# Kernel optimization log

Measured on AMD Instinct MI355X. Metric: run time of the kernel, lower is better.

Reference implementation:

```python
import jax, jax.numpy as jnp
import numpy as np


def setup_inputs() -> dict:
    key = jax.random.key(0)
    k1, k2 = jax.random.split(key)
    B, N, D, OUT = 4, 8192, 64, 64
    inputs = jax.random.normal(k1, (B, N, D), dtype=jnp.float32)
    kernel = jax.random.normal(k2, (D, OUT), dtype=jnp.float32) * (1.0 / np.sqrt(D))
    return {"inputs": inputs, "kernel": kernel}


def reference(inputs, kernel):
    # sim = X X^T  -> [B, N, N] dense similarity (unscaled self-attention, V = X)
    sim = jnp.einsum("bnd,bmd->bnm", inputs, inputs)
    A = jax.nn.softmax(sim, axis=-1)          # row-wise softmax over neighbors
    h = jnp.einsum("bnm,bmd->bnd", A, inputs)  # aggregate
    return jnp.einsum("bnd,do->bno", h, kernel)  # output projection
```

## Files before the change

### kernel.cpp

```cpp
#include <hip/hip_runtime.h>
#include <math.h>

typedef _Float16 f16;
typedef _Float16 f16x2 __attribute__((ext_vector_type(2)));
typedef _Float16 f16x4 __attribute__((ext_vector_type(4)));
typedef _Float16 f16x8 __attribute__((ext_vector_type(8)));
typedef float    f32x4 __attribute__((ext_vector_type(4)));

#define PKRTZ(a, b) __builtin_bit_cast(f16x2, __builtin_amdgcn_cvt_pkrtz((a), (b)))

#define NN 8192
#define DD 64
#define KT 32
#define NQB 64
#define NWAVES 4
#define KPW (NN / NWAVES)
#define NTILES (KPW / KT)

#define LOG2E 1.44269504088896f

__global__ __launch_bounds__(256, 2)
void prep_f16(const float* __restrict__ X, f16* __restrict__ Xn, f16* __restrict__ Xv)
{
  __shared__ f16 Lt[64 * 72];
  const int tid  = threadIdx.x;
  const int b    = blockIdx.x >> 7;
  const int kb64 = (blockIdx.x & 127) * 64;

  {
    const int r = tid >> 2;
    const int c = (tid & 3) * 16;
    const float* p = X + ((size_t)(b * NN + kb64 + r)) * DD + c;
    const float4 a0 = *(const float4*)(p);
    const float4 a1 = *(const float4*)(p + 4);
    const float4 a2 = *(const float4*)(p + 8);
    const float4 a3 = *(const float4*)(p + 12);
    f16x8 v0, v1;
    v0[0]=(f16)a0.x; v0[1]=(f16)a0.y; v0[2]=(f16)a0.z; v0[3]=(f16)a0.w;
    v0[4]=(f16)a1.x; v0[5]=(f16)a1.y; v0[6]=(f16)a1.z; v0[7]=(f16)a1.w;
    v1[0]=(f16)a2.x; v1[1]=(f16)a2.y; v1[2]=(f16)a2.z; v1[3]=(f16)a2.w;
    v1[4]=(f16)a3.x; v1[5]=(f16)a3.y; v1[6]=(f16)a3.z; v1[7]=(f16)a3.w;
    f16* dn = Xn + ((size_t)(b * NN + kb64 + r)) * DD + c;
    *(f16x8*)(dn)     = v0;
    *(f16x8*)(dn + 8) = v1;
    *(f16x8*)&Lt[r * 72 + c]     = v0;
    *(f16x8*)&Lt[r * 72 + c + 8] = v1;
  }
  __syncthreads();
  {
    const int h  = tid >> 7;
    const int r  = tid & 127;
    const int jh = r & 1;
    const int d  = r >> 1;
    union { f16 s[16]; f16x8 v[2]; } u;
    #pragma unroll
    for (int j = 0; j < 16; ++j) u.s[j] = Lt[(h * 32 + jh * 16 + j) * 72 + d];
    const int kt = (kb64 >> 5) + h;
    f16* dst = Xv + (((size_t)(b * (NN / 32) + kt)) * DD + d) * 32 + jh * 16;
    *(f16x8*)&dst[0] = u.v[0];
    *(f16x8*)&dst[8] = u.v[1];
  }
}

#define P_PITCH 36
#define P_HALF  (64 * P_PITCH)
#define P_BYTES (2 * P_HALF * 2)
#define HL_PITCH 68
#define WL_OFF  (64 * HL_PITCH * 4)
#define LST_OFF (2 * 64 * HL_PITCH * 4)
#define SMEM_B  (NWAVES * P_BYTES)

__global__ __launch_bounds__(256, 2)
void gconv_attn(const float* __restrict__ X, const f16* __restrict__ Xn,
                const f16* __restrict__ Xv, const float* __restrict__ W,
                float* __restrict__ out)
{
  __shared__ __align__(16) unsigned char smem[SMEM_B];

  const int tid  = threadIdx.x;
  const int lane = tid & 63;
  const int wave = tid >> 6;
  const int q15  = lane & 15;
  const int quad = lane >> 4;

  const int xcd   = blockIdx.x & 7;
  const int slot  = blockIdx.x >> 3;
  const int batch = xcd >> 1;
  const int qblk  = slot * 2 + (xcd & 1);
  const int qbase = qblk * NQB;
  const float* Xb = X + (size_t)batch * NN * DD;

  f16* PwA = (f16*)(smem + wave * P_BYTES);
  f16* PwB = PwA + P_HALF;

  const f16* XnW = Xn + ((size_t)batch * NN + wave * KPW) * DD + q15 * DD + quad * 8;
  const f16* XvW = Xv + (((size_t)batch * (NN / 32) + wave * NTILES)) * DD * 32
                      + q15 * 32 + quad * 8;

  f16x8 qf[4][2];
  f32x4 minit[4];
  float lrow[4];
  #pragma unroll
  for (int qt = 0; qt < 4; ++qt) {
    const float* qp = Xb + (size_t)(qbase + qt*16 + q15) * DD + quad*8;
    float nrm = 0.f;
    #pragma unroll
    for (int c = 0; c < 2; ++c) {
      const float4 a = *(const float4*)(qp + c*32);
      const float4 b = *(const float4*)(qp + c*32 + 4);
      float xs[8] = {a.x, a.y, a.z, a.w, b.x, b.y, b.z, b.w};
      f16x8 v;
      #pragma unroll
      for (int e = 0; e < 8; ++e) {
        const f16 kv = (f16)xs[e];
        const f16 qs = (f16)(xs[e] * LOG2E);
        nrm += (float)qs * (float)kv;
        v[e] = qs;
      }
      qf[qt][c] = v;
    }
    nrm += __shfl_xor(nrm, 16);
    nrm += __shfl_xor(nrm, 32);
    const float m2 = nrm + 2.0f;
    minit[qt] = (f32x4){-m2, -m2, -m2, -m2};
    lrow[qt] = 0.f;
  }

  f32x4 acc[4][4];
  #pragma unroll
  for (int a = 0; a < 4; ++a)
    #pragma unroll
    for (int b = 0; b < 4; ++b)
      acc[a][b] = (f32x4){0.f, 0.f, 0.f, 0.f};

  const f16x2 kOnes = (f16x2){(f16)1.0f, (f16)1.0f};

  f16x8 ka[2][2], vbA[4], vbB[4];
  f32x4 sqk[4][2];

  auto LDK = [&](int t) {
    const f16* kn = XnW + (size_t)t * (KT * DD);
    #pragma unroll
    for (int g = 0; g < 2; ++g)
      #pragma unroll
      for (int c = 0; c < 2; ++c)
        ka[g][c] = *(const f16x8*)(kn + g * 16 * DD + c * 32);
  };
  auto LDV = [&](f16x8 (&vb)[4], int t) {
    const f16* vn = XvW + (size_t)t * (DD * 32);
    #pragma unroll
    for (int mt = 0; mt < 4; ++mt)
      vb[mt] = *(const f16x8*)(vn + mt * 16 * 32);
  };
  auto QK = [&]() {
    #pragma unroll
    for (int qt = 0; qt < 4; ++qt)
      #pragma unroll
      for (int g = 0; g < 2; ++g) {
        f32x4 s = __builtin_amdgcn_mfma_f32_16x16x32_f16(ka[g][0], qf[qt][0], minit[qt], 0, 0, 0);
        sqk[qt][g] = __builtin_amdgcn_mfma_f32_16x16x32_f16(ka[g][1], qf[qt][1], s, 0, 0, 0);
      }
  };
  auto SM = [&](f16* Pd) {
    #pragma unroll
    for (int qt = 0; qt < 4; ++qt)
      #pragma unroll
      for (int g = 0; g < 2; ++g) {
        const float p0 = __builtin_amdgcn_exp2f(sqk[qt][g][0]);
        const float p1 = __builtin_amdgcn_exp2f(sqk[qt][g][1]);
        const float p2 = __builtin_amdgcn_exp2f(sqk[qt][g][2]);
        const float p3 = __builtin_amdgcn_exp2f(sqk[qt][g][3]);
        union { f16x4 v; f16x2 h[2]; } pu;
        pu.h[0] = PKRTZ(p0, p1);
        pu.h[1] = PKRTZ(p2, p3);
        lrow[qt] = __builtin_amdgcn_fdot2(pu.h[0], kOnes, lrow[qt], false);
        lrow[qt] = __builtin_amdgcn_fdot2(pu.h[1], kOnes, lrow[qt], false);
        *(f16x4*)&Pd[(qt*16 + q15)*P_PITCH + g*16 + quad*4] = pu.v;
      }
  };
  auto PV = [&](const f16x8 (&vb)[4], const f16* Ps) {
    #pragma unroll
    for (int qt = 0; qt < 4; ++qt) {
      union { f16x8 v; f16x4 h[2]; } pu;
      pu.h[0] = *(const f16x4*)&Ps[(qt*16 + q15)*P_PITCH + quad*8];
      pu.h[1] = *(const f16x4*)&Ps[(qt*16 + q15)*P_PITCH + quad*8 + 4];
      #pragma unroll
      for (int mt = 0; mt < 4; ++mt)
        acc[qt][mt] = __builtin_amdgcn_mfma_f32_16x16x32_f16(vb[mt], pu.v, acc[qt][mt], 0, 0, 0);
    }
  };

  LDK(0);
  LDV(vbA, 0);
  QK();
  LDK(1);
  SM(PwA);
  LDV(vbB, 1);

  for (int t = 1; t < NTILES - 1; t += 2) {
    QK();
    LDK(t + 1);
    PV(vbA, PwA);
    LDV(vbA, t + 1);
    SM(PwB);
    QK();
    LDK(t + 2);
    PV(vbB, PwB);
    LDV(vbB, t + 2);
    SM(PwA);
  }

  QK();
  PV(vbA, PwA);
  SM(PwB);
  PV(vbB, PwB);

  __syncthreads();
  float* Hl    = (float*)smem;
  float* Wl    = (float*)(smem + WL_OFF);
  float* Lstar = (float*)(smem + LST_OFF);

  for (int i = tid; i < 64*HL_PITCH; i += 256) Hl[i] = 0.f;
  for (int i = tid; i < 64*64; i += 256) Wl[(i >> 6)*HL_PITCH + (i & 63)] = W[i];
  if (tid < 64) Lstar[tid] = 0.f;
  __syncthreads();

  #pragma unroll
  for (int qt = 0; qt < 4; ++qt) {
    float lr = lrow[qt];
    lr += __shfl_xor(lr, 16);
    lr += __shfl_xor(lr, 32);
    if (quad == 0) atomicAdd(&Lstar[qt*16 + q15], lr);
    #pragma unroll
    for (int mt = 0; mt < 4; ++mt)
      #pragma unroll
      for (int rr = 0; rr < 4; ++rr)
        atomicAdd(&Hl[(mt*16 + quad*4 + rr)*HL_PITCH + qt*16 + q15], acc[qt][mt][rr]);
  }
  __syncthreads();

  {
    const int qq = tid >> 2;
    const int og = (tid & 3) * 16;
    f32x4 o[4];
    #pragma unroll
    for (int i = 0; i < 4; ++i) o[i] = (f32x4){0.f,0.f,0.f,0.f};
    for (int d = 0; d < 64; ++d) {
      const float h = Hl[d*HL_PITCH + qq];
      const f32x4* wr = (const f32x4*)&Wl[d*HL_PITCH + og];
      #pragma unroll
      for (int i = 0; i < 4; ++i) o[i] += h * wr[i];
    }
    const float inv = 1.0f / Lstar[qq];
    float* op = out + ((size_t)batch * NN + qbase + qq) * DD + og;
    #pragma unroll
    for (int i = 0; i < 4; ++i)
      *(f32x4*)(op + i*4) = o[i] * inv;
  }
}

extern "C" void kernel_launch(void* const* d_in, const int* in_sizes, int n_in,
                              void* d_out, int out_size, void* d_ws, size_t ws_size,
                              hipStream_t stream) {
  const float* X = (const float*)d_in[0];
  const float* W = (const float*)d_in[1];
  float* out = (float*)d_out;

  f16* Xn = (f16*)d_ws;
  f16* Xv = (f16*)((char*)d_ws + (size_t)4 * NN * DD * 2);
  prep_f16<<<dim3(512), dim3(256), 0, stream>>>(X, Xn, Xv);
  gconv_attn<<<dim3(512), dim3(256), 0, stream>>>(X, Xn, Xv, W, out);
}
```

Baseline: 203.8 us.

## Switch attention to 32x32x16 MFMA and pass P in registers

The attention loop now uses 32x32x16 MFMA tiles instead of 16x16x32. The prep kernel permutes key rows within each 32-row group, so the QK^T output layout lines up with the A-operand layout of the PV MFMA. That lets the softmax probabilities feed the PV MFMA straight from registers, which removes the per-wave shared-memory P buffers and their LDS writes and reads. The explicit two-stage software pipeline is replaced by a simpler single-tile prefetch loop, which gives up some overlap between the QK, exp and PV phases. It also adds register pressure from the 16-wide accumulators under a 2-blocks-per-CU launch bound.

```diff
diff --git a/kernel.cpp b/kernel.cpp
--- a/kernel.cpp
+++ b/kernel.cpp
@@ -5,9 +5,11 @@
 typedef _Float16 f16x2 __attribute__((ext_vector_type(2)));
 typedef _Float16 f16x4 __attribute__((ext_vector_type(4)));
 typedef _Float16 f16x8 __attribute__((ext_vector_type(8)));
-typedef float    f32x4 __attribute__((ext_vector_type(4)));
+typedef float    f32x4  __attribute__((ext_vector_type(4)));
+typedef float    f32x16 __attribute__((ext_vector_type(16)));
 
 #define PKRTZ(a, b) __builtin_bit_cast(f16x2, __builtin_amdgcn_cvt_pkrtz((a), (b)))
+#define MFMA32(a, b, c) __builtin_amdgcn_mfma_f32_32x32x16_f16((a), (b), (c), 0, 0, 0)
 
 #define NN 8192
 #define DD 64
@@ -19,6 +21,11 @@
 
 #define LOG2E 1.44269504088896f
 
+__device__ __forceinline__ int sig32(int k) {
+  const int g = (k >> 2) & 3;
+  return (g == 1 || g == 2) ? (k ^ 12) : k;
+}
+
 __global__ __launch_bounds__(256, 2)
 void prep_f16(const float* __restrict__ X, f16* __restrict__ Xn, f16* __restrict__ Xv)
 {
@@ -28,8 +35,9 @@
   const int kb64 = (blockIdx.x & 127) * 64;
 
   {
-    const int r = tid >> 2;
-    const int c = (tid & 3) * 16;
+    const int r  = tid >> 2;
+    const int rr = (r & 32) | sig32(r & 31);
+    const int c  = (tid & 3) * 16;
     const float* p = X + ((size_t)(b * NN + kb64 + r)) * DD + c;
     const float4 a0 = *(const float4*)(p);
     const float4 a1 = *(const float4*)(p + 4);
@@ -40,7 +48,7 @@
     v0[4]=(f16)a1.x; v0[5]=(f16)a1.y; v0[6]=(f16)a1.z; v0[7]=(f16)a1.w;
     v1[0]=(f16)a2.x; v1[1]=(f16)a2.y; v1[2]=(f16)a2.z; v1[3]=(f16)a2.w;
     v1[4]=(f16)a3.x; v1[5]=(f16)a3.y; v1[6]=(f16)a3.z; v1[7]=(f16)a3.w;
-    f16* dn = Xn + ((size_t)(b * NN + kb64 + r)) * DD + c;
+    f16* dn = Xn + ((size_t)(b * NN + kb64 + rr)) * DD + c;
     *(f16x8*)(dn)     = v0;
     *(f16x8*)(dn + 8) = v1;
     *(f16x8*)&Lt[r * 72 + c]     = v0;
@@ -62,13 +70,10 @@
   }
 }
 
-#define P_PITCH 36
-#define P_HALF  (64 * P_PITCH)
-#define P_BYTES (2 * P_HALF * 2)
 #define HL_PITCH 68
 #define WL_OFF  (64 * HL_PITCH * 4)
 #define LST_OFF (2 * 64 * HL_PITCH * 4)
-#define SMEM_B  (NWAVES * P_BYTES)
+#define SMEM_B  (LST_OFF + 64 * 4)
 
 __global__ __launch_bounds__(256, 2)
 void gconv_attn(const float* __restrict__ X, const f16* __restrict__ Xn,
@@ -80,8 +85,8 @@
   const int tid  = threadIdx.x;
   const int lane = tid & 63;
   const int wave = tid >> 6;
-  const int q15  = lane & 15;
-  const int quad = lane >> 4;
+  const int l31  = lane & 31;
+  const int hi   = lane >> 5;
 
   const int xcd   = blockIdx.x & 7;
   const int slot  = blockIdx.x >> 3;
@@ -90,24 +95,21 @@
   const int qbase = qblk * NQB;
   const float* Xb = X + (size_t)batch * NN * DD;
 
-  f16* PwA = (f16*)(smem + wave * P_BYTES);
-  f16* PwB = PwA + P_HALF;
-
-  const f16* XnW = Xn + ((size_t)batch * NN + wave * KPW) * DD + q15 * DD + quad * 8;
-  const f16* XvW = Xv + (((size_t)batch * (NN / 32) + wave * NTILES)) * DD * 32
-                      + q15 * 32 + quad * 8;
-
-  f16x8 qf[4][2];
-  f32x4 minit[4];
-  float lrow[4];
+  const f16* XnW = Xn + ((size_t)batch * NN + wave * KPW) * DD + l31 * DD + hi * 8;
+  const f16* XvW = Xv + ((size_t)batch * (NN / 32) + wave * NTILES) * (DD * 32)
+                      + l31 * 32 + hi * 8;
+
+  f16x8 qf[2][4];
+  f32x16 minit[2];
+  float lrow[2];
   #pragma unroll
-  for (int qt = 0; qt < 4; ++qt) {
-    const float* qp = Xb + (size_t)(qbase + qt*16 + q15) * DD + quad*8;
+  for (int qb = 0; qb < 2; ++qb) {
+    const float* qp = Xb + (size_t)(qbase + qb*32 + l31) * DD + hi*8;
     float nrm = 0.f;
     #pragma unroll
-    for (int c = 0; c < 2; ++c) {
-      const float4 a = *(const float4*)(qp + c*32);
-      const float4 b = *(const float4*)(qp + c*32 + 4);
+    for (int c = 0; c < 4; ++c) {
+      const float4 a = *(const float4*)(qp + c*16);
+      const float4 b = *(const float4*)(qp + c*16 + 4);
       float xs[8] = {a.x, a.y, a.z, a.w, b.x, b.y, b.z, b.w};
       f16x8 v;
       #pragma unroll
@@ -117,103 +119,91 @@
         nrm += (float)qs * (float)kv;
         v[e] = qs;
       }
-      qf[qt][c] = v;
+      qf[qb][c] = v;
     }
-    nrm += __shfl_xor(nrm, 16);
     nrm += __shfl_xor(nrm, 32);
     const float m2 = nrm + 2.0f;
-    minit[qt] = (f32x4){-m2, -m2, -m2, -m2};
-    lrow[qt] = 0.f;
-  }
-
-  f32x4 acc[4][4];
+    #pragma unroll
+    for (int e = 0; e < 16; ++e) minit[qb][e] = -m2;
+    lrow[qb] = 0.f;
+  }
+
+  f32x16 acc[2][2];
   #pragma unroll
-  for (int a = 0; a < 4; ++a)
-    #pragma unroll
-    for (int b = 0; b < 4; ++b)
-      acc[a][b] = (f32x4){0.f, 0.f, 0.f, 0.f};
+  for (int a = 0; a < 2; ++a)
+    #pragma unroll
+    for (int b = 0; b < 2; ++b)
+      #pragma unroll
+      for (int e = 0; e < 16; ++e) acc[a][b][e] = 0.f;
 
   const f16x2 kOnes = (f16x2){(f16)1.0f, (f16)1.0f};
 
-  f16x8 ka[2][2], vbA[4], vbB[4];
-  f32x4 sqk[4][2];
+  f16x8 ka[4];
+  f16x8 vb[2][2];
 
   auto LDK = [&](int t) {
     const f16* kn = XnW + (size_t)t * (KT * DD);
     #pragma unroll
-    for (int g = 0; g < 2; ++g)
-      #pragma unroll
-      for (int c = 0; c < 2; ++c)
-        ka[g][c] = *(const f16x8*)(kn + g * 16 * DD + c * 32);
+    for (int c = 0; c < 4; ++c)
+      ka[c] = *(const f16x8*)(kn + c * 16);
   };
-  auto LDV = [&](f16x8 (&vb)[4], int t) {
+  auto LDV = [&](int t) {
     const f16* vn = XvW + (size_t)t * (DD * 32);
     #pragma unroll
-    for (int mt = 0; mt < 4; ++mt)
-      vb[mt] = *(const f16x8*)(vn + mt * 16 * 32);
+    for (int db = 0; db < 2; ++db)
+      #pragma unroll
+      for (int kh = 0; kh < 2; ++kh)
+        vb[db][kh] = *(const f16x8*)(vn + db * 1024 + kh * 16);
   };
-  auto QK = [&]() {
-    #pragma unroll
-    for (int qt = 0; qt < 4; ++qt)
-      #pragma unroll
-      for (int g = 0; g < 2; ++g) {
-        f32x4 s = __builtin_amdgcn_mfma_f32_16x16x32_f16(ka[g][0], qf[qt][0], minit[qt], 0, 0, 0);
-        sqk[qt][g] = __builtin_amdgcn_mfma_f32_16x16x32_f16(ka[g][1], qf[qt][1], s, 0, 0, 0);
-      }
+
+  auto SMpack = [&](const f32x16& s, float& lr, f16x8& paLo, f16x8& paHi) {
+    float p[16];
+    #pragma unroll
+    for (int r = 0; r < 16; ++r) p[r] = __builtin_amdgcn_exp2f(s[r]);
+    union { f16x8 v; f16x2 h[4]; } a, b;
+    a.h[0] = PKRTZ(p[0],  p[1]);  a.h[1] = PKRTZ(p[2],  p[3]);
+    a.h[2] = PKRTZ(p[4],  p[5]);  a.h[3] = PKRTZ(p[6],  p[7]);
+    b.h[0] = PKRTZ(p[8],  p[9]);  b.h[1] = PKRTZ(p[10], p[11]);
+    b.h[2] = PKRTZ(p[12], p[13]); b.h[3] = PKRTZ(p[14], p[15]);
+    #pragma unroll
+    for (int i = 0; i < 4; ++i) {
+      lr = __builtin_amdgcn_fdot2(a.h[i], kOnes, lr, false);
+      lr = __builtin_amdgcn_fdot2(b.h[i], kOnes, lr, false);
+    }
+    paLo = a.v; paHi = b.v;
   };
-  auto SM = [&](f16* Pd) {
-    #pragma unroll
-    for (int qt = 0; qt < 4; ++qt)
-      #pragma unroll
-      for (int g = 0; g < 2; ++g) {
-        const float p0 = __builtin_amdgcn_exp2f(sqk[qt][g][0]);
-        const float p1 = __builtin_amdgcn_exp2f(sqk[qt][g][1]);
-        const float p2 = __builtin_amdgcn_exp2f(sqk[qt][g][2]);
-        const float p3 = __builtin_amdgcn_exp2f(sqk[qt][g][3]);
-        union { f16x4 v; f16x2 h[2]; } pu;
-        pu.h[0] = PKRTZ(p0, p1);
-        pu.h[1] = PKRTZ(p2, p3);
-        lrow[qt] = __builtin_amdgcn_fdot2(pu.h[0], kOnes, lrow[qt], false);
-        lrow[qt] = __builtin_amdgcn_fdot2(pu.h[1], kOnes, lrow[qt], false);
-        *(f16x4*)&Pd[(qt*16 + q15)*P_PITCH + g*16 + quad*4] = pu.v;
-      }
-  };
-  auto PV = [&](const f16x8 (&vb)[4], const f16* Ps) {
-    #pragma unroll
-    for (int qt = 0; qt < 4; ++qt) {
-      union { f16x8 v; f16x4 h[2]; } pu;
-      pu.h[0] = *(const f16x4*)&Ps[(qt*16 + q15)*P_PITCH + quad*8];
-      pu.h[1] = *(const f16x4*)&Ps[(qt*16 + q15)*P_PITCH + quad*8 + 4];
-      #pragma unroll
-      for (int mt = 0; mt < 4; ++mt)
-        acc[qt][mt] = __builtin_amdgcn_mfma_f32_16x16x32_f16(vb[mt], pu.v, acc[qt][mt], 0, 0, 0);
-    }
-  };
 
   LDK(0);
-  LDV(vbA, 0);
-  QK();
-  LDK(1);
-  SM(PwA);
-  LDV(vbB, 1);
-
-  for (int t = 1; t < NTILES - 1; t += 2) {
-    QK();
-    LDK(t + 1);
-    PV(vbA, PwA);
-    LDV(vbA, t + 1);
-    SM(PwB);
-    QK();
-    LDK(t + 2);
-    PV(vbB, PwB);
-    LDV(vbB, t + 2);
-    SM(PwA);
-  }
-
-  QK();
-  PV(vbA, PwA);
-  SM(PwB);
-  PV(vbB, PwB);
+  LDV(0);
+  for (int t = 0; t < NTILES; ++t) {
+    const int tn = (t + 1 < NTILES) ? t + 1 : t;
+
+    f32x16 s0 = MFMA32(ka[0], qf[0][0], minit[0]);
+    s0 = MFMA32(ka[1], qf[0][1], s0);
+    s0 = MFMA32(ka[2], qf[0][2], s0);
+    s0 = MFMA32(ka[3], qf[0][3], s0);
+    f32x16 s1 = MFMA32(ka[0], qf[1][0], minit[1]);
+    s1 = MFMA32(ka[1], qf[1][1], s1);
+    s1 = MFMA32(ka[2], qf[1][2], s1);
+    s1 = MFMA32(ka[3], qf[1][3], s1);
+
+    LDK(tn);
+
+    f16x8 pa00, pa01, pa10, pa11;
+    SMpack(s0, lrow[0], pa00, pa01);
+    SMpack(s1, lrow[1], pa10, pa11);
+
+    acc[0][0] = MFMA32(pa00, vb[0][0], acc[0][0]);
+    acc[0][0] = MFMA32(pa01, vb[0][1], acc[0][0]);
+    acc[0][1] = MFMA32(pa00, vb[1][0], acc[0][1]);
+    acc[0][1] = MFMA32(pa01, vb[1][1], acc[0][1]);
+    acc[1][0] = MFMA32(pa10, vb[0][0], acc[1][0]);
+    acc[1][0] = MFMA32(pa11, vb[0][1], acc[1][0]);
+    acc[1][1] = MFMA32(pa10, vb[1][0], acc[1][1]);
+    acc[1][1] = MFMA32(pa11, vb[1][1], acc[1][1]);
+
+    LDV(tn);
+  }
 
   __syncthreads();
   float* Hl    = (float*)smem;
@@ -226,16 +216,17 @@
   __syncthreads();
 
   #pragma unroll
-  for (int qt = 0; qt < 4; ++qt) {
-    float lr = lrow[qt];
-    lr += __shfl_xor(lr, 16);
+  for (int qb = 0; qb < 2; ++qb) {
+    float lr = lrow[qb];
     lr += __shfl_xor(lr, 32);
-    if (quad == 0) atomicAdd(&Lstar[qt*16 + q15], lr);
-    #pragma unroll
-    for (int mt = 0; mt < 4; ++mt)
-      #pragma unroll
-      for (int rr = 0; rr < 4; ++rr)
-        atomicAdd(&Hl[(mt*16 + quad*4 + rr)*HL_PITCH + qt*16 + q15], acc[qt][mt][rr]);
+    if (lane < 32) atomicAdd(&Lstar[qb*32 + lane], lr);
+    #pragma unroll
+    for (int db = 0; db < 2; ++db)
+      #pragma unroll
+      for (int r = 0; r < 16; ++r) {
+        const int ql = (r & 3) + 8*(r >> 2) + 4*hi;
+        atomicAdd(&Hl[(db*32 + l31)*HL_PITCH + qb*32 + ql], acc[qb][db][r]);
+      }
   }
   __syncthreads();
 
```

Result: no change. 204.7 us (+0.5%).
